# Kernel tuning notes

Hardware: AMD Instinct MI355X
Metric: run time of the kernel (lower is better)

The kernel has to match this reference:

```python
import jax, jax.numpy as jnp
import numpy as np
import math

N, LQ, LK = 4, 2048, 2048
H, P = 16, 64
D = H * P  # 1024
EPS = 1e-5


def setup_inputs() -> dict:
    key = jax.random.key(0)
    ks = jax.random.split(key, 5)
    s = 1.0 / math.sqrt(D)
    return {
        "query": jax.random.normal(ks[0], (N, LQ, D), dtype=jnp.float32),
        "key": jax.random.normal(ks[1], (N, LK, D), dtype=jnp.float32),
        "Wq": jax.random.normal(ks[2], (D, D), dtype=jnp.float32) * s,
        "Wk": jax.random.normal(ks[3], (D, D), dtype=jnp.float32) * s,
        "Wv": jax.random.normal(ks[4], (D, D), dtype=jnp.float32) * s,
        "gamma": jnp.ones((D,), dtype=jnp.float32),
        "beta": jnp.zeros((D,), dtype=jnp.float32),
    }


def reference(query, key, Wq, Wk, Wv, gamma, beta):
    n, lq, _ = query.shape
    lk = key.shape[1]
    # Linear projections (torch Linear: x @ W.T), reshaped into heads
    q = (query @ Wq.T).reshape(n, lq, H, P)
    k = (key @ Wk.T).reshape(n, lk, H, P)
    v = (key @ Wv.T).reshape(n, lk, H, P)
    # score: (N, Lq, Lk, H), scaled by sqrt(out_channels)=sqrt(D)
    score = jnp.einsum("nqhp,nkhp->nqkh", q, k) / math.sqrt(D)
    # causal mask: triu(ones, diagonal=1) -> masked positions set to -1e6
    causal = jnp.triu(jnp.ones((lq, lk), dtype=bool), k=1)
    score = jnp.where(causal[None, :, :, None], jnp.float32(-1000000.0), score)
    attention = jax.nn.softmax(score, axis=2)  # softmax over key dim
    res = jnp.einsum("nqkh,nkhp->nqhp", attention, v).reshape(n, lq, D)
    res = res + query
    # BatchNorm0d over flattened (N*Lq, D), training-mode batch statistics
    flat = res.reshape(-1, D)
    mean = jnp.mean(flat, axis=0)
    var = jnp.var(flat, axis=0)  # biased variance, as torch BN normalization
    flat = (flat - mean) / jnp.sqrt(var + EPS) * gamma + beta
    return flat.reshape(n, lq, D)
```

## Files before the change

### kernel.cpp

```cpp
#include <hip/hip_runtime.h>
#include <hip/hip_bf16.h>

typedef __attribute__((ext_vector_type(8))) short short8;
typedef __attribute__((ext_vector_type(4))) short short4v;
typedef __attribute__((ext_vector_type(4))) float float4v;

#define LQN 2048
#define DM 1024

#define GAS __attribute__((address_space(1)))
#define LAS __attribute__((address_space(3)))

__device__ __forceinline__ short f2bf(float f) {
  unsigned u = __builtin_bit_cast(unsigned, f);
  u += 0x7fff + ((u >> 16) & 1);
  return (short)(u >> 16);
}

__device__ __forceinline__ float4v mfma_pv(short4v a, short4v b, float4v c) {
#if defined(__HIP_DEVICE_COMPILE__)
#if __has_builtin(__builtin_amdgcn_mfma_f32_16x16x16_bf16)
  return __builtin_amdgcn_mfma_f32_16x16x16_bf16(a, b, c, 0, 0, 0);
#else
  return __builtin_amdgcn_mfma_f32_16x16x16bf16_1k(a, b, c, 0, 0, 0);
#endif
#else
  (void)a; (void)b;
  return c;
#endif
}

__global__ __launch_bounds__(256) void convert_qk(const float* __restrict__ q,
                                                  const float* __restrict__ k,
                                                  short* __restrict__ dst0)
{
  const float* src = blockIdx.y ? k : q;
  short* dst = dst0 + (size_t)blockIdx.y * 8388608;
  const size_t base = ((size_t)blockIdx.x * 256 + threadIdx.x) * 8;
  float4v a = *(const float4v*)&src[base];
  float4v b = *(const float4v*)&src[base + 4];
  short8 o8 = {f2bf(a.x), f2bf(a.y), f2bf(a.z), f2bf(a.w),
               f2bf(b.x), f2bf(b.y), f2bf(b.z), f2bf(b.w)};
  *(short8*)&dst[base] = o8;
}

__global__ __launch_bounds__(256) void convert_w(const float* __restrict__ Wq,
                                                 const float* __restrict__ Wk,
                                                 const float* __restrict__ Wv,
                                                 short* __restrict__ Wbf)
{
  const int z = blockIdx.y;
  const float* src = (z == 0) ? Wq : (z == 1) ? Wk : Wv;
  short* dst = Wbf + (size_t)z * 1048576;
  const size_t base = ((size_t)blockIdx.x * 256 + threadIdx.x) * 8;
  float4v a = *(const float4v*)&src[base];
  float4v b = *(const float4v*)&src[base + 4];
  short8 o8 = {f2bf(a.x), f2bf(a.y), f2bf(a.z), f2bf(a.w),
               f2bf(b.x), f2bf(b.y), f2bf(b.z), f2bf(b.w)};
  *(short8*)&dst[base] = o8;
}

template <bool WBF>
__global__ __launch_bounds__(256, 2) void gemm_qkv(
    const short* __restrict__ Abf, const float* __restrict__ Wq,
    const float* __restrict__ Wk, const float* __restrict__ Wv,
    const short* __restrict__ Wbf,
    short* __restrict__ Qbf, short* __restrict__ Kbf, short* __restrict__ Vt)
{
  __shared__ __align__(16) short As[128 * 32];
  __shared__ __align__(16) short Bs[128 * (WBF ? 32 : 40)];
  constexpr int LDB = WBF ? 32 : 40;

  const int z = blockIdx.z;
  const short* Ag = (z == 0) ? Abf : (Abf + 8388608);
  const float* Wg = (z == 0) ? Wq : (z == 1) ? Wk : Wv;
  const short* Wbz = WBF ? (Wbf + (size_t)z * 1048576) : nullptr;

  const int m0 = blockIdx.x * 128;
  const int n0 = blockIdx.y * 128;
  const int t = threadIdx.x;
  const int lane = t & 63;
  const int lrow = lane & 15;
  const int quad = lane >> 4;
  const int wave = t >> 6;
  const int wm = (wave & 1) * 64;
  const int wn = (wave >> 1) * 64;

  float4v acc[4][4];
#pragma unroll
  for (int i = 0; i < 4; i++)
#pragma unroll
    for (int j = 0; j < 4; j++) acc[i][j] = (float4v){0.f, 0.f, 0.f, 0.f};

  for (int kk = 0; kk < 1024; kk += 32) {
    __syncthreads();
#pragma unroll
    for (int p = 0; p < 2; p++) {
      const int c = p * 256 + t;
      const int row = c >> 2, qg = c & 3;
      const short* gp = &Ag[(size_t)(m0 + row) * DM + kk + qg * 8];
      short* lp = &As[(p * 256 + (t & 192)) * 8];
      __builtin_amdgcn_global_load_lds((const GAS void*)gp, (LAS void*)lp, 16, 0, 0);
      if (WBF) {
        const short* gpb = &Wbz[(size_t)(n0 + row) * DM + kk + qg * 8];
        short* lpb = &Bs[(p * 256 + (t & 192)) * 8];
        __builtin_amdgcn_global_load_lds((const GAS void*)gpb, (LAS void*)lpb, 16, 0, 0);
      }
    }
    if (!WBF) {
#pragma unroll
      for (int p = 0; p < 4; p++) {
        const int row = p * 32 + (t >> 3);
        const int sc = (t & 7) * 4;
        float4v b = *(const float4v*)&Wg[(size_t)(n0 + row) * DM + kk + sc];
        short4v b16 = {f2bf(b.x), f2bf(b.y), f2bf(b.z), f2bf(b.w)};
        *(short4v*)&Bs[row * LDB + sc] = b16;
      }
    }
    __syncthreads();

    short8 af[4], bf[4];
#pragma unroll
    for (int i = 0; i < 4; i++) {
      af[i] = *(const short8*)&As[(wm + i * 16 + lrow) * 32 + quad * 8];
      bf[i] = *(const short8*)&Bs[(wn + i * 16 + lrow) * LDB + quad * 8];
    }
#pragma unroll
    for (int i = 0; i < 4; i++)
#pragma unroll
      for (int j = 0; j < 4; j++)
        acc[i][j] = __builtin_amdgcn_mfma_f32_16x16x32_bf16(af[i], bf[j],
                                                            acc[i][j], 0, 0, 0);
  }

  if (z < 2) {
    short* Og = (z == 0) ? Qbf : Kbf;
    const float sc = (z == 0) ? 0.03125f : 1.0f;
#pragma unroll
    for (int i = 0; i < 4; i++)
#pragma unroll
      for (int j = 0; j < 4; j++)
#pragma unroll
        for (int r = 0; r < 4; r++) {
          const int row = m0 + wm + i * 16 + quad * 4 + r;
          const int col = n0 + wn + j * 16 + lrow;
          Og[(size_t)row * DM + col] = f2bf(acc[i][j][r] * sc);
        }
  } else {
#pragma unroll
    for (int i = 0; i < 4; i++) {
      const int rowb = m0 + wm + i * 16 + quad * 4;
      const int batch = rowb >> 11;
      const int kpos = rowb & 2047;
#pragma unroll
      for (int j = 0; j < 4; j++) {
        const int col = n0 + wn + j * 16 + lrow;
        short4v pk = {f2bf(acc[i][j][0]), f2bf(acc[i][j][1]),
                      f2bf(acc[i][j][2]), f2bf(acc[i][j][3])};
        *(short4v*)&Vt[(size_t)batch * DM * LQN + (size_t)col * LQN + kpos] = pk;
      }
    }
  }
}

__global__ __launch_bounds__(256, 4) void flash_attn(
    const short* __restrict__ Qbf, const short* __restrict__ Kbf,
    const short* __restrict__ Vt, const float* __restrict__ query,
    float* __restrict__ res)
{
  __shared__ __align__(16) short Ks[2][4096];
  __shared__ __align__(16) short Vs[2][64 * 76];

  const int b = blockIdx.x;
  const int nh = (b & 7) | ((b >> 7) << 3);
  const int qt = (b >> 3) & 15;
  const int h = nh & 15;
  const int n = nh >> 4;
  const int t = threadIdx.x;
  const int lane = t & 63;
  const int wave = t >> 6;
  const int lrow = lane & 15;
  const int quad = lane >> 4;

  const size_t rowoff = (size_t)n * LQN;
  const size_t hcol = (size_t)h * 64;
  const size_t vtoff = (size_t)n * (size_t)DM * LQN + hcol * LQN;

  const int qb = qt * 128;
  const int wrow = qb + wave * 32;

  short8 qf[2][2];
#pragma unroll
  for (int mt = 0; mt < 2; mt++)
#pragma unroll
    for (int dh = 0; dh < 2; dh++)
      qf[mt][dh] = *(const short8*)
          &Qbf[(rowoff + wrow + mt * 16 + lrow) * DM + hcol + dh * 32 + quad * 8];

  float4v o[2][4];
#pragma unroll
  for (int mt = 0; mt < 2; mt++)
#pragma unroll
    for (int j = 0; j < 4; j++) o[mt][j] = (float4v){0.f, 0.f, 0.f, 0.f};
  float lsum[2] = {0.f, 0.f};

  const int nkt = 2 * qt + 2;

  const int skey = t >> 2;
  const int sq8 = (t & 3) * 8;
  const int skq = (t & 3) * 16;
  const int ldsbase = (t & 192) * 8;

  {
    const short* g0 = &Kbf[(rowoff + skey) * DM + hcol + sq8];
    __builtin_amdgcn_global_load_lds((const GAS void*)g0,
                                     (LAS void*)&Ks[0][ldsbase], 16, 0, 0);
    const short* g1 = &Kbf[(rowoff + skey) * DM + hcol + 32 + sq8];
    __builtin_amdgcn_global_load_lds((const GAS void*)g1,
                                     (LAS void*)&Ks[0][2048 + ldsbase], 16, 0, 0);
    const short* gv = &Vt[vtoff + (size_t)skey * LQN + skq];
    short4v v0 = *(const short4v*)(gv);
    short4v v1 = *(const short4v*)(gv + 4);
    short4v v2 = *(const short4v*)(gv + 8);
    short4v v3 = *(const short4v*)(gv + 12);
    short* l = &Vs[0][skey * 76 + skq];
    *(short4v*)(l + 0) = v0;
    *(short4v*)(l + 4) = v1;
    *(short4v*)(l + 8) = v2;
    *(short4v*)(l + 12) = v3;
  }

  for (int kt = 0; kt < nkt; kt++) {
    __syncthreads();
    const int buf = kt & 1;
    const int nbuf = buf ^ 1;
    const int kbase = kt * 64;
    const bool more = (kt + 1 < nkt);

    short4v v0, v1, v2, v3;
    if (more) {
      const int kb2 = kbase + 64;
      const short* g0 = &Kbf[(rowoff + kb2 + skey) * DM + hcol + sq8];
      __builtin_amdgcn_global_load_lds((const GAS void*)g0,
                                       (LAS void*)&Ks[nbuf][ldsbase], 16, 0, 0);
      const short* g1 = &Kbf[(rowoff + kb2 + skey) * DM + hcol + 32 + sq8];
      __builtin_amdgcn_global_load_lds((const GAS void*)g1,
                                       (LAS void*)&Ks[nbuf][2048 + ldsbase], 16, 0, 0);
      const short* gv = &Vt[vtoff + (size_t)skey * LQN + kb2 + skq];
      v0 = *(const short4v*)(gv);
      v1 = *(const short4v*)(gv + 4);
      v2 = *(const short4v*)(gv + 8);
      v3 = *(const short4v*)(gv + 12);
    }

    const int drel = wrow - kbase;
#pragma unroll
    for (int f4 = 0; f4 < 4; f4++) {
      if (f4 * 16 > drel + 31) continue;
      short8 kf0 = *(const short8*)&Ks[buf][(f4 * 16 + lrow) * 32 + quad * 8];
      short8 kf1 = *(const short8*)&Ks[buf][2048 + (f4 * 16 + lrow) * 32 + quad * 8];
      short4v vf[4];
#pragma unroll
      for (int j = 0; j < 4; j++)
        vf[j] = *(const short4v*)&Vs[buf][(j * 16 + lrow) * 76 + f4 * 16 + quad * 4];
#pragma unroll
      for (int mt = 0; mt < 2; mt++) {
        if (f4 * 16 > drel + mt * 16 + 15) continue;
        float4v z = (float4v){0.f, 0.f, 0.f, 0.f};
        z = __builtin_amdgcn_mfma_f32_16x16x32_bf16(kf0, qf[mt][0], z, 0, 0, 0);
        z = __builtin_amdgcn_mfma_f32_16x16x32_bf16(kf1, qf[mt][1], z, 0, 0, 0);
        const bool pm = (f4 * 16 + 15 > drel + mt * 16);
        const int dk = drel + mt * 16 + lrow;
        short4v pk;
        float ls = 0.f;
#pragma unroll
        for (int r = 0; r < 4; r++) {
          float p = __expf(z[r]);
          if (pm && (f4 * 16 + quad * 4 + r > dk)) p = 0.f;
          ls += p;
          pk[r] = f2bf(p);
        }
        lsum[mt] += ls;
#pragma unroll
        for (int j = 0; j < 4; j++)
          o[mt][j] = mfma_pv(pk, vf[j], o[mt][j]);
      }
    }

    if (more) {
      short* l = &Vs[nbuf][skey * 76 + skq];
      *(short4v*)(l + 0) = v0;
      *(short4v*)(l + 4) = v1;
      *(short4v*)(l + 8) = v2;
      *(short4v*)(l + 12) = v3;
    }
  }

  float inv[2][4];
#pragma unroll
  for (int mt = 0; mt < 2; mt++) {
    float s = lsum[mt];
    s += __shfl_xor(s, 16);
    s += __shfl_xor(s, 32);
#pragma unroll
    for (int r = 0; r < 4; r++) inv[mt][r] = 1.0f / __shfl(s, quad * 4 + r);
  }

#pragma unroll
  for (int mt = 0; mt < 2; mt++)
#pragma unroll
    for (int r = 0; r < 4; r++) {
      const size_t row = rowoff + wrow + mt * 16 + quad * 4 + r;
#pragma unroll
      for (int j = 0; j < 4; j++) {
        const size_t idx = row * DM + hcol + j * 16 + lrow;
        res[idx] = o[mt][j][r] * inv[mt][r] + query[idx];
      }
    }
}

__global__ __launch_bounds__(256) void bn_stats(const float* __restrict__ res,
                                                float* __restrict__ stats)
{
  const int t = threadIdx.x;
  const int b = blockIdx.x;
  float4v sum = (float4v){0.f, 0.f, 0.f, 0.f};
  float4v sq = (float4v){0.f, 0.f, 0.f, 0.f};
  for (int r = 0; r < 32; r++) {
    float4v v = *(const float4v*)&res[(size_t)(b * 32 + r) * DM + t * 4];
    sum += v;
    sq += v * v;
  }
#pragma unroll
  for (int i = 0; i < 4; i++) {
    atomicAdd(&stats[t * 4 + i], sum[i]);
    atomicAdd(&stats[1024 + t * 4 + i], sq[i]);
  }
}

__global__ __launch_bounds__(256) void bn_apply(float* __restrict__ res,
                                                const float* __restrict__ stats,
                                                const float* __restrict__ gamma,
                                                const float* __restrict__ beta)
{
  const size_t i = (size_t)blockIdx.x * 256 + threadIdx.x;
  const int c = (int)(i & 255) * 4;
  float4v v = *(const float4v*)&res[i * 4];
  float4v sm = *(const float4v*)&stats[c];
  float4v sq = *(const float4v*)&stats[1024 + c];
  float4v g = *(const float4v*)&gamma[c];
  float4v bt = *(const float4v*)&beta[c];
  float4v outv;
#pragma unroll
  for (int j = 0; j < 4; j++) {
    const float mean = sm[j] * (1.0f / 8192.0f);
    const float var = sq[j] * (1.0f / 8192.0f) - mean * mean;
    outv[j] = (v[j] - mean) * rsqrtf(var + 1e-5f) * g[j] + bt[j];
  }
  *(float4v*)&res[i * 4] = outv;
}

extern "C" void kernel_launch(void* const* d_in, const int* in_sizes, int n_in,
                              void* d_out, int out_size, void* d_ws,
                              size_t ws_size, hipStream_t stream)
{
  const float* query = (const float*)d_in[0];
  const float* key   = (const float*)d_in[1];
  const float* Wq    = (const float*)d_in[2];
  const float* Wk    = (const float*)d_in[3];
  const float* Wv    = (const float*)d_in[4];
  const float* gamma = (const float*)d_in[5];
  const float* beta  = (const float*)d_in[6];
  float* out = (float*)d_out;

  char* ws = (char*)d_ws;
  short* Qbf = (short*)(ws);
  short* Kbf = (short*)(ws + (size_t)16 * 1024 * 1024);
  short* Vt  = (short*)(ws + (size_t)32 * 1024 * 1024);
  float* stats = (float*)(ws + (size_t)48 * 1024 * 1024);
  short* Wbf = (short*)(ws + (size_t)49 * 1024 * 1024);
  const bool wbf = ws_size >= ((size_t)55 << 20);

  (void)hipMemsetAsync(stats, 0, 2048 * sizeof(float), stream);

  convert_qk<<<dim3(4096, 2), 256, 0, stream>>>(query, key, (short*)d_out);
  if (wbf) {
    convert_w<<<dim3(512, 3), 256, 0, stream>>>(Wq, Wk, Wv, Wbf);
    gemm_qkv<true><<<dim3(64, 8, 3), 256, 0, stream>>>(
        (const short*)d_out, Wq, Wk, Wv, Wbf, Qbf, Kbf, Vt);
  } else {
    gemm_qkv<false><<<dim3(64, 8, 3), 256, 0, stream>>>(
        (const short*)d_out, Wq, Wk, Wv, nullptr, Qbf, Kbf, Vt);
  }
  flash_attn<<<dim3(1024), 256, 0, stream>>>(Qbf, Kbf, Vt, query, out);
  bn_stats<<<dim3(256), 256, 0, stream>>>(out, stats);
  bn_apply<<<dim3(8192), 256, 0, stream>>>(out, stats, gamma, beta);
}
```

Baseline: 329.8 us.

## Pair causal query tiles per block, deepen GEMM K-step, use exp2 softmax

The flash attention kernel now gives each block two query tiles (qt and 15-qt), so every block does the same amount of causal work and the grid shrinks to 512 blocks. The QKV GEMM processes 64 K-columns per sync using two 32-wide LDS planes, which halves the number of barriers. The log2(e) factor is folded into the Q scale so the softmax can use exp2f instead of __expf. bn_stats reads 16 rows per block over 512 blocks instead of 32 rows over 256. The risks are less parallelism in attention, since each block handles two tiles in sequence, and the larger LDS footprint in the GEMM.

Result: slower. 345.2 us (+4.7%).

```diff
diff --git a/kernel.cpp b/kernel.cpp
--- a/kernel.cpp
+++ b/kernel.cpp
@@ -67,9 +67,8 @@
     const short* __restrict__ Wbf,
     short* __restrict__ Qbf, short* __restrict__ Kbf, short* __restrict__ Vt)
 {
-  __shared__ __align__(16) short As[128 * 32];
-  __shared__ __align__(16) short Bs[128 * (WBF ? 32 : 40)];
-  constexpr int LDB = WBF ? 32 : 40;
+  __shared__ __align__(16) short As[2 * 4096];
+  __shared__ __align__(16) short Bs[2 * 4096];
 
   const int z = blockIdx.z;
   const short* Ag = (z == 0) ? Abf : (Abf + 8388608);
@@ -86,56 +85,68 @@
   const int wm = (wave & 1) * 64;
   const int wn = (wave >> 1) * 64;
 
+  const int srow = t >> 2;
+  const int scol8 = (t & 3) * 8;
+  const int sldsb = (t & 192) * 8;
+
   float4v acc[4][4];
 #pragma unroll
   for (int i = 0; i < 4; i++)
 #pragma unroll
     for (int j = 0; j < 4; j++) acc[i][j] = (float4v){0.f, 0.f, 0.f, 0.f};
 
-  for (int kk = 0; kk < 1024; kk += 32) {
+  for (int kk = 0; kk < 1024; kk += 64) {
     __syncthreads();
 #pragma unroll
-    for (int p = 0; p < 2; p++) {
-      const int c = p * 256 + t;
-      const int row = c >> 2, qg = c & 3;
-      const short* gp = &Ag[(size_t)(m0 + row) * DM + kk + qg * 8];
-      short* lp = &As[(p * 256 + (t & 192)) * 8];
-      __builtin_amdgcn_global_load_lds((const GAS void*)gp, (LAS void*)lp, 16, 0, 0);
-      if (WBF) {
-        const short* gpb = &Wbz[(size_t)(n0 + row) * DM + kk + qg * 8];
-        short* lpb = &Bs[(p * 256 + (t & 192)) * 8];
-        __builtin_amdgcn_global_load_lds((const GAS void*)gpb, (LAS void*)lpb, 16, 0, 0);
+    for (int pl = 0; pl < 2; pl++) {
+#pragma unroll
+      for (int q = 0; q < 2; q++) {
+        const int row = q * 64 + srow;
+        const short* gp = &Ag[(size_t)(m0 + row) * DM + kk + pl * 32 + scol8];
+        short* lp = &As[pl * 4096 + (q * 256 + (t & 192)) * 8];
+        __builtin_amdgcn_global_load_lds((const GAS void*)gp, (LAS void*)lp, 16, 0, 0);
+        if (WBF) {
+          const short* gpb = &Wbz[(size_t)(n0 + row) * DM + kk + pl * 32 + scol8];
+          short* lpb = &Bs[pl * 4096 + (q * 256 + (t & 192)) * 8];
+          __builtin_amdgcn_global_load_lds((const GAS void*)gpb, (LAS void*)lpb, 16, 0, 0);
+        }
       }
     }
     if (!WBF) {
 #pragma unroll
       for (int p = 0; p < 4; p++) {
         const int row = p * 32 + (t >> 3);
-        const int sc = (t & 7) * 4;
-        float4v b = *(const float4v*)&Wg[(size_t)(n0 + row) * DM + kk + sc];
-        short4v b16 = {f2bf(b.x), f2bf(b.y), f2bf(b.z), f2bf(b.w)};
-        *(short4v*)&Bs[row * LDB + sc] = b16;
+#pragma unroll
+        for (int cp = 0; cp < 2; cp++) {
+          const int c4 = (t & 7) * 4;
+          float4v b = *(const float4v*)&Wg[(size_t)(n0 + row) * DM + kk + cp * 32 + c4];
+          short4v b16 = {f2bf(b.x), f2bf(b.y), f2bf(b.z), f2bf(b.w)};
+          *(short4v*)&Bs[cp * 4096 + row * 32 + c4] = b16;
+        }
       }
     }
     __syncthreads();
 
-    short8 af[4], bf[4];
-#pragma unroll
-    for (int i = 0; i < 4; i++) {
-      af[i] = *(const short8*)&As[(wm + i * 16 + lrow) * 32 + quad * 8];
-      bf[i] = *(const short8*)&Bs[(wn + i * 16 + lrow) * LDB + quad * 8];
-    }
-#pragma unroll
-    for (int i = 0; i < 4; i++)
-#pragma unroll
-      for (int j = 0; j < 4; j++)
-        acc[i][j] = __builtin_amdgcn_mfma_f32_16x16x32_bf16(af[i], bf[j],
-                                                            acc[i][j], 0, 0, 0);
+#pragma unroll
+    for (int ko = 0; ko < 2; ko++) {
+      short8 af[4], bf[4];
+#pragma unroll
+      for (int i = 0; i < 4; i++) {
+        af[i] = *(const short8*)&As[ko * 4096 + (wm + i * 16 + lrow) * 32 + quad * 8];
+        bf[i] = *(const short8*)&Bs[ko * 4096 + (wn + i * 16 + lrow) * 32 + quad * 8];
+      }
+#pragma unroll
+      for (int i = 0; i < 4; i++)
+#pragma unroll
+        for (int j = 0; j < 4; j++)
+          acc[i][j] = __builtin_amdgcn_mfma_f32_16x16x32_bf16(af[i], bf[j],
+                                                              acc[i][j], 0, 0, 0);
+    }
   }
 
   if (z < 2) {
     short* Og = (z == 0) ? Qbf : Kbf;
-    const float sc = (z == 0) ? 0.03125f : 1.0f;
+    const float sc = (z == 0) ? 0.03125f * 1.44269504f : 1.0f;
 #pragma unroll
     for (int i = 0; i < 4; i++)
 #pragma unroll
@@ -172,8 +183,8 @@
   __shared__ __align__(16) short Vs[2][64 * 76];
 
   const int b = blockIdx.x;
-  const int nh = (b & 7) | ((b >> 7) << 3);
-  const int qt = (b >> 3) & 15;
+  const int nh = (b & 7) | ((b >> 6) << 3);
+  const int pair = (b >> 3) & 7;
   const int h = nh & 15;
   const int n = nh >> 4;
   const int t = threadIdx.x;
@@ -186,137 +197,141 @@
   const size_t hcol = (size_t)h * 64;
   const size_t vtoff = (size_t)n * (size_t)DM * LQN + hcol * LQN;
 
-  const int qb = qt * 128;
-  const int wrow = qb + wave * 32;
-
-  short8 qf[2][2];
-#pragma unroll
-  for (int mt = 0; mt < 2; mt++)
-#pragma unroll
-    for (int dh = 0; dh < 2; dh++)
-      qf[mt][dh] = *(const short8*)
-          &Qbf[(rowoff + wrow + mt * 16 + lrow) * DM + hcol + dh * 32 + quad * 8];
-
-  float4v o[2][4];
-#pragma unroll
-  for (int mt = 0; mt < 2; mt++)
-#pragma unroll
-    for (int j = 0; j < 4; j++) o[mt][j] = (float4v){0.f, 0.f, 0.f, 0.f};
-  float lsum[2] = {0.f, 0.f};
-
-  const int nkt = 2 * qt + 2;
-
   const int skey = t >> 2;
   const int sq8 = (t & 3) * 8;
   const int skq = (t & 3) * 16;
   const int ldsbase = (t & 192) * 8;
 
-  {
-    const short* g0 = &Kbf[(rowoff + skey) * DM + hcol + sq8];
-    __builtin_amdgcn_global_load_lds((const GAS void*)g0,
-                                     (LAS void*)&Ks[0][ldsbase], 16, 0, 0);
-    const short* g1 = &Kbf[(rowoff + skey) * DM + hcol + 32 + sq8];
-    __builtin_amdgcn_global_load_lds((const GAS void*)g1,
-                                     (LAS void*)&Ks[0][2048 + ldsbase], 16, 0, 0);
-    const short* gv = &Vt[vtoff + (size_t)skey * LQN + skq];
-    short4v v0 = *(const short4v*)(gv);
-    short4v v1 = *(const short4v*)(gv + 4);
-    short4v v2 = *(const short4v*)(gv + 8);
-    short4v v3 = *(const short4v*)(gv + 12);
-    short* l = &Vs[0][skey * 76 + skq];
-    *(short4v*)(l + 0) = v0;
-    *(short4v*)(l + 4) = v1;
-    *(short4v*)(l + 8) = v2;
-    *(short4v*)(l + 12) = v3;
-  }
-
-  for (int kt = 0; kt < nkt; kt++) {
-    __syncthreads();
-    const int buf = kt & 1;
-    const int nbuf = buf ^ 1;
-    const int kbase = kt * 64;
-    const bool more = (kt + 1 < nkt);
-
-    short4v v0, v1, v2, v3;
-    if (more) {
-      const int kb2 = kbase + 64;
-      const short* g0 = &Kbf[(rowoff + kb2 + skey) * DM + hcol + sq8];
+#pragma unroll
+  for (int half = 0; half < 2; half++) {
+    const int qt = half ? (15 - pair) : pair;
+    const int qb = qt * 128;
+    const int wrow = qb + wave * 32;
+
+    short8 qf[2][2];
+#pragma unroll
+    for (int mt = 0; mt < 2; mt++)
+#pragma unroll
+      for (int dh = 0; dh < 2; dh++)
+        qf[mt][dh] = *(const short8*)
+            &Qbf[(rowoff + wrow + mt * 16 + lrow) * DM + hcol + dh * 32 + quad * 8];
+
+    float4v o[2][4];
+#pragma unroll
+    for (int mt = 0; mt < 2; mt++)
+#pragma unroll
+      for (int j = 0; j < 4; j++) o[mt][j] = (float4v){0.f, 0.f, 0.f, 0.f};
+    float lsum[2] = {0.f, 0.f};
+
+    const int nkt = 2 * qt + 2;
+
+    {
+      const short* g0 = &Kbf[(rowoff + skey) * DM + hcol + sq8];
       __builtin_amdgcn_global_load_lds((const GAS void*)g0,
-                                       (LAS void*)&Ks[nbuf][ldsbase], 16, 0, 0);
-      const short* g1 = &Kbf[(rowoff + kb2 + skey) * DM + hcol + 32 + sq8];
+                                       (LAS void*)&Ks[0][ldsbase], 16, 0, 0);
+      const short* g1 = &Kbf[(rowoff + skey) * DM + hcol + 32 + sq8];
       __builtin_amdgcn_global_load_lds((const GAS void*)g1,
-                                       (LAS void*)&Ks[nbuf][2048 + ldsbase], 16, 0, 0);
-      const short* gv = &Vt[vtoff + (size_t)skey * LQN + kb2 + skq];
-      v0 = *(const short4v*)(gv);
-      v1 = *(const short4v*)(gv + 4);
-      v2 = *(const short4v*)(gv + 8);
-      v3 = *(const short4v*)(gv + 12);
-    }
-
-    const int drel = wrow - kbase;
-#pragma unroll
-    for (int f4 = 0; f4 < 4; f4++) {
-      if (f4 * 16 > drel + 31) continue;
-      short8 kf0 = *(const short8*)&Ks[buf][(f4 * 16 + lrow) * 32 + quad * 8];
-      short8 kf1 = *(const short8*)&Ks[buf][2048 + (f4 * 16 + lrow) * 32 + quad * 8];
-      short4v vf[4];
-#pragma unroll
-      for (int j = 0; j < 4; j++)
-        vf[j] = *(const short4v*)&Vs[buf][(j * 16 + lrow) * 76 + f4 * 16 + quad * 4];
-#pragma unroll
-      for (int mt = 0; mt < 2; mt++) {
-        if (f4 * 16 > drel + mt * 16 + 15) continue;
-        float4v z = (float4v){0.f, 0.f, 0.f, 0.f};
-        z = __builtin_amdgcn_mfma_f32_16x16x32_bf16(kf0, qf[mt][0], z, 0, 0, 0);
-        z = __builtin_amdgcn_mfma_f32_16x16x32_bf16(kf1, qf[mt][1], z, 0, 0, 0);
-        const bool pm = (f4 * 16 + 15 > drel + mt * 16);
-        const int dk = drel + mt * 16 + lrow;
-        short4v pk;
-        float ls = 0.f;
-#pragma unroll
-        for (int r = 0; r < 4; r++) {
-          float p = __expf(z[r]);
-          if (pm && (f4 * 16 + quad * 4 + r > dk)) p = 0.f;
-          ls += p;
-          pk[r] = f2bf(p);
-        }
-        lsum[mt] += ls;
-#pragma unroll
-        for (int j = 0; j < 4; j++)
-          o[mt][j] = mfma_pv(pk, vf[j], o[mt][j]);
-      }
-    }
-
-    if (more) {
-      short* l = &Vs[nbuf][skey * 76 + skq];
+                                       (LAS void*)&Ks[0][2048 + ldsbase], 16, 0, 0);
+      const short* gv = &Vt[vtoff + (size_t)skey * LQN + skq];
+      short4v v0 = *(const short4v*)(gv);
+      short4v v1 = *(const short4v*)(gv + 4);
+      short4v v2 = *(const short4v*)(gv + 8);
+      short4v v3 = *(const short4v*)(gv + 12);
+      short* l = &Vs[0][skey * 76 + skq];
       *(short4v*)(l + 0) = v0;
       *(short4v*)(l + 4) = v1;
       *(short4v*)(l + 8) = v2;
       *(short4v*)(l + 12) = v3;
     }
-  }
-
-  float inv[2][4];
-#pragma unroll
-  for (int mt = 0; mt < 2; mt++) {
-    float s = lsum[mt];
-    s += __shfl_xor(s, 16);
-    s += __shfl_xor(s, 32);
-#pragma unroll
-    for (int r = 0; r < 4; r++) inv[mt][r] = 1.0f / __shfl(s, quad * 4 + r);
-  }
-
-#pragma unroll
-  for (int mt = 0; mt < 2; mt++)
-#pragma unroll
-    for (int r = 0; r < 4; r++) {
-      const size_t row = rowoff + wrow + mt * 16 + quad * 4 + r;
-#pragma unroll
-      for (int j = 0; j < 4; j++) {
-        const size_t idx = row * DM + hcol + j * 16 + lrow;
-        res[idx] = o[mt][j][r] * inv[mt][r] + query[idx];
-      }
-    }
+
+    for (int kt = 0; kt < nkt; kt++) {
+      __syncthreads();
+      const int buf = kt & 1;
+      const int nbuf = buf ^ 1;
+      const int kbase = kt * 64;
+      const bool more = (kt + 1 < nkt);
+
+      short4v v0, v1, v2, v3;
+      if (more) {
+        const int kb2 = kbase + 64;
+        const short* g0 = &Kbf[(rowoff + kb2 + skey) * DM + hcol + sq8];
+        __builtin_amdgcn_global_load_lds((const GAS void*)g0,
+                                         (LAS void*)&Ks[nbuf][ldsbase], 16, 0, 0);
+        const short* g1 = &Kbf[(rowoff + kb2 + skey) * DM + hcol + 32 + sq8];
+        __builtin_amdgcn_global_load_lds((const GAS void*)g1,
+                                         (LAS void*)&Ks[nbuf][2048 + ldsbase], 16, 0, 0);
+        const short* gv = &Vt[vtoff + (size_t)skey * LQN + kb2 + skq];
+        v0 = *(const short4v*)(gv);
+        v1 = *(const short4v*)(gv + 4);
+        v2 = *(const short4v*)(gv + 8);
+        v3 = *(const short4v*)(gv + 12);
+      }
+
+      const int drel = wrow - kbase;
+#pragma unroll
+      for (int f4 = 0; f4 < 4; f4++) {
+        if (f4 * 16 > drel + 31) continue;
+        short8 kf0 = *(const short8*)&Ks[buf][(f4 * 16 + lrow) * 32 + quad * 8];
+        short8 kf1 = *(const short8*)&Ks[buf][2048 + (f4 * 16 + lrow) * 32 + quad * 8];
+        short4v vf[4];
+#pragma unroll
+        for (int j = 0; j < 4; j++)
+          vf[j] = *(const short4v*)&Vs[buf][(j * 16 + lrow) * 76 + f4 * 16 + quad * 4];
+#pragma unroll
+        for (int mt = 0; mt < 2; mt++) {
+          if (f4 * 16 > drel + mt * 16 + 15) continue;
+          float4v z = (float4v){0.f, 0.f, 0.f, 0.f};
+          z = __builtin_amdgcn_mfma_f32_16x16x32_bf16(kf0, qf[mt][0], z, 0, 0, 0);
+          z = __builtin_amdgcn_mfma_f32_16x16x32_bf16(kf1, qf[mt][1], z, 0, 0, 0);
+          const bool pm = (f4 * 16 + 15 > drel + mt * 16);
+          const int dk = drel + mt * 16 + lrow;
+          short4v pk;
+          float ls = 0.f;
+#pragma unroll
+          for (int r = 0; r < 4; r++) {
+            float p = exp2f(z[r]);
+            if (pm && (f4 * 16 + quad * 4 + r > dk)) p = 0.f;
+            ls += p;
+            pk[r] = f2bf(p);
+          }
+          lsum[mt] += ls;
+#pragma unroll
+          for (int j = 0; j < 4; j++)
+            o[mt][j] = mfma_pv(pk, vf[j], o[mt][j]);
+        }
+      }
+
+      if (more) {
+        short* l = &Vs[nbuf][skey * 76 + skq];
+        *(short4v*)(l + 0) = v0;
+        *(short4v*)(l + 4) = v1;
+        *(short4v*)(l + 8) = v2;
+        *(short4v*)(l + 12) = v3;
+      }
+    }
+
+    float inv[2][4];
+#pragma unroll
+    for (int mt = 0; mt < 2; mt++) {
+      float s = lsum[mt];
+      s += __shfl_xor(s, 16);
+      s += __shfl_xor(s, 32);
+#pragma unroll
+      for (int r = 0; r < 4; r++) inv[mt][r] = 1.0f / __shfl(s, quad * 4 + r);
+    }
+
+#pragma unroll
+    for (int mt = 0; mt < 2; mt++)
+#pragma unroll
+      for (int r = 0; r < 4; r++) {
+        const size_t row = rowoff + wrow + mt * 16 + quad * 4 + r;
+#pragma unroll
+        for (int j = 0; j < 4; j++) {
+          const size_t idx = row * DM + hcol + j * 16 + lrow;
+          res[idx] = o[mt][j][r] * inv[mt][r] + query[idx];
+        }
+      }
+  }
 }
 
 __global__ __launch_bounds__(256) void bn_stats(const float* __restrict__ res,
@@ -326,8 +341,8 @@
   const int b = blockIdx.x;
   float4v sum = (float4v){0.f, 0.f, 0.f, 0.f};
   float4v sq = (float4v){0.f, 0.f, 0.f, 0.f};
-  for (int r = 0; r < 32; r++) {
-    float4v v = *(const float4v*)&res[(size_t)(b * 32 + r) * DM + t * 4];
+  for (int r = 0; r < 16; r++) {
+    float4v v = *(const float4v*)&res[(size_t)(b * 16 + r) * DM + t * 4];
     sum += v;
     sq += v * v;
   }
@@ -392,7 +407,7 @@
     gemm_qkv<false><<<dim3(64, 8, 3), 256, 0, stream>>>(
         (const short*)d_out, Wq, Wk, Wv, nullptr, Qbf, Kbf, Vt);
   }
-  flash_attn<<<dim3(1024), 256, 0, stream>>>(Qbf, Kbf, Vt, query, out);
-  bn_stats<<<dim3(256), 256, 0, stream>>>(out, stats);
+  flash_attn<<<dim3(512), 256, 0, stream>>>(Qbf, Kbf, Vt, query, out);
+  bn_stats<<<dim3(512), 256, 0, stream>>>(out, stats);
   bn_apply<<<dim3(8192), 256, 0, stream>>>(out, stats, gamma, beta);
 }
```
